# Kernel optimization log

Measured on AMD Instinct MI355X. Metric: run time of the kernel, lower is better.

The kernel has to match this reference:

```python
import jax, jax.numpy as jnp
import numpy as np

N = 50000      # nodes
E = 800000     # edges (avg degree 16)
DIN = 128
DH = 128
DOUT = 8


def setup_inputs() -> dict:
    key = jax.random.key(0)
    ks = jax.random.split(key, 9)
    def lin(k, o, i):
        return (jax.random.normal(k, (o, i), jnp.float32) / np.sqrt(i)).astype(jnp.float32)
    return {
        "x": jax.random.normal(ks[0], (N, DIN), jnp.float32),
        "edge_index": jax.random.randint(ks[1], (2, E), 0, N),
        "edge_attr": jax.random.normal(ks[2], (E, 1), jnp.float32),
        # SAGEConv params: lin_l (applied to mean-aggregated neighbors, with bias)
        # and lin_r (applied to root node, no bias), per PyG defaults.
        "W1l": lin(ks[3], DH, DIN), "b1l": jnp.zeros((DH,), jnp.float32), "W1r": lin(ks[4], DH, DIN),
        "Whl": lin(ks[5], DH, DH),  "bhl": jnp.zeros((DH,), jnp.float32), "Whr": lin(ks[6], DH, DH),
        "W2l": lin(ks[7], DOUT, DH), "b2l": jnp.zeros((DOUT,), jnp.float32), "W2r": lin(ks[8], DOUT, DH),
    }


def _sage_conv(x, src, dst, Wl, bl, Wr, n):
    # mean aggregation of source features onto destination nodes
    s = jax.ops.segment_sum(x[src], dst, num_segments=n)              # [N, d]
    c = jax.ops.segment_sum(jnp.ones((src.shape[0],), x.dtype), dst, num_segments=n)
    agg = s / jnp.maximum(c, 1.0)[:, None]
    return agg @ Wl.T + bl + x @ Wr.T


def reference(x, edge_index, edge_attr, W1l, b1l, W1r, Whl, bhl, Whr, W2l, b2l, W2r):
    # edge_attr is accepted but unused, matching the original forward.
    src, dst = edge_index[0], edge_index[1]
    n = x.shape[0]
    h = jax.nn.relu(_sage_conv(x, src, dst, W1l, b1l, W1r, n))
    # dropout p=0.5 is identity at inference (training=False)
    h = jax.nn.elu(_sage_conv(h, src, dst, Whl, bhl, Whr, n))
    h = _sage_conv(h, src, dst, W2l, b2l, W2r, n)
    return jax.nn.log_softmax(h, axis=1)
```

## Files before the change

### kernel.cpp

```cpp
#include <hip/hip_runtime.h>

typedef unsigned int u32;
typedef unsigned short u16;
typedef short bf16x8 __attribute__((ext_vector_type(8)));
typedef float f32x4 __attribute__((ext_vector_type(4)));

#define NCB 256

__device__ __forceinline__ float bf2f(u16 h) { return __uint_as_float(((u32)h) << 16); }
__device__ __forceinline__ u16 f2bf(float f) {
    u32 u = __float_as_uint(f);
    return (u16)((u + 0x7fffu + ((u >> 16) & 1u)) >> 16);
}

__global__ __launch_bounds__(256) void k_sentinel(u16* out, int n) {
    int i = blockIdx.x * 256 + threadIdx.x;
    if (i < n) out[i] = f2bf(-7.0f);
}

__global__ void k_detect(const u32* x, int* flag) {
    int lane = threadIdx.x;
    int c = 0;
    for (int j = 0; j < 4; ++j) {
        u32 u = x[lane * 4 + j];
        u32 e = (u >> 7) & 0xffu;
        if ((e >= 0x30u && e <= 0x47u) || ((u & 0x7fffu) == 0u)) ++c;
    }
    for (int d = 32; d; d >>= 1) c += __shfl_down(c, d, 64);
    if (lane == 0) *flag = (c < 128) ? 1 : 0;
}

__global__ __launch_bounds__(256) void k_front(
    const void* x, const int* dstv, const int* flag, int bucketed,
    uint4* X, int* C, int E, int N, int chunk, int cvtB,
    const void* s1l, const void* s1r, const void* shl, const void* shr,
    const void* s2l, const void* s2r, const void* sb1, const void* sbh,
    const void* sb2,
    u32* w1l, u32* w1r, u32* whl, u32* whr, u32* w2l, u32* w2r,
    float* bf1, float* bfh, float* bf2) {
    __shared__ int hist[256];
    int b = blockIdx.x, t = threadIdx.x;
    if (b < cvtB) {
        int i = b * 256 + t;
        if (i >= N * 16) return;
        if (*flag) {
            const float4* s = (const float4*)x;
            float4 a = s[2 * i], c4 = s[2 * i + 1];
            uint4 o;
            o.x = (u32)f2bf(a.x) | ((u32)f2bf(a.y) << 16);
            o.y = (u32)f2bf(a.z) | ((u32)f2bf(a.w) << 16);
            o.z = (u32)f2bf(c4.x) | ((u32)f2bf(c4.y) << 16);
            o.w = (u32)f2bf(c4.z) | ((u32)f2bf(c4.w) << 16);
            X[i] = o;
        } else {
            X[i] = ((const uint4*)x)[i];
        }
    } else if (b < cvtB + 134) {
        int bb = b - cvtB;
        int fl = *flag;
        auto cv = [&](const void* src, u32* dst, int base) {
            int i = base + t;
            if (fl) {
                const float* s = (const float*)src;
                dst[i] = (u32)f2bf(s[2 * i]) | ((u32)f2bf(s[2 * i + 1]) << 16);
            } else {
                dst[i] = ((const u32*)src)[i];
            }
        };
        auto cb = [&](const void* src, float* dst, int i) {
            dst[i] = fl ? ((const float*)src)[i] : bf2f(((const u16*)src)[i]);
        };
        if      (bb <  32) cv(s1l, w1l, bb * 256);
        else if (bb <  64) cv(s1r, w1r, (bb - 32) * 256);
        else if (bb <  96) cv(shl, whl, (bb - 64) * 256);
        else if (bb < 128) cv(shr, whr, (bb - 96) * 256);
        else if (bb < 130) cv(s2l, w2l, (bb - 128) * 256);
        else if (bb < 132) cv(s2r, w2r, (bb - 130) * 256);
        else if (bb == 132) {
            if (t < 128) cb(sb1, bf1, t);
            else         cb(sbh, bfh, t - 128);
        } else {
            if (t < 8) cb(sb2, bf2, t);
        }
    } else if (bucketed) {
        int cb2 = b - cvtB - 134;
        hist[t] = 0;
        __syncthreads();
        int e0 = cb2 * chunk;
        int e1 = min(e0 + chunk, E);
        for (int e = e0 + t; e < e1; e += 256) {
            int d = min(max(dstv[e], 0), N - 1);
            atomicAdd(&hist[d >> 8], 1);
        }
        __syncthreads();
        C[cb2 * 256 + t] = hist[t];
    }
}

__global__ __launch_bounds__(256) void k_scanT(int* C, int* T) {
    __shared__ int sm[256];
    int bu = blockIdx.x, t = threadIdx.x;
    int v = C[t * 256 + bu];
    sm[t] = v;
    __syncthreads();
    for (int off = 1; off < 256; off <<= 1) {
        int u = (t >= off) ? sm[t - off] : 0;
        __syncthreads();
        sm[t] += u;
        __syncthreads();
    }
    C[t * 256 + bu] = sm[t] - v;
    if (t == 255) T[bu] = sm[255];
}

__global__ __launch_bounds__(256) void k_scanB(const int* T, int* B, int nbuk) {
    __shared__ int sm[256];
    int t = threadIdx.x;
    int v = (t < nbuk) ? T[t] : 0;
    sm[t] = v;
    __syncthreads();
    for (int off = 1; off < 256; off <<= 1) {
        int u = (t >= off) ? sm[t - off] : 0;
        __syncthreads();
        sm[t] += u;
        __syncthreads();
    }
    B[t] = sm[t] - v;
}

__global__ __launch_bounds__(256) void k_place(const int* srcv, const int* dstv,
                                               const int* C, const int* Bb,
                                               u32* pairs, int E, int N, int chunk) {
    __shared__ int base[256], cnt[256];
    int t = threadIdx.x;
    base[t] = Bb[t] + C[blockIdx.x * 256 + t];
    cnt[t] = 0;
    __syncthreads();
    int e0 = blockIdx.x * chunk;
    int e1 = min(e0 + chunk, E);
    for (int e = e0 + t; e < e1; e += 256) {
        int d = min(max(dstv[e], 0), N - 1);
        int s = min(max(srcv[e], 0), N - 1);
        int b = d >> 8;
        int pos = base[b] + atomicAdd(&cnt[b], 1);
        pos = min(max(pos, 0), E - 1);
        pairs[pos] = ((u32)s << 8) | (u32)(d & 255);
    }
}

__global__ __launch_bounds__(256) void k_fillb2(const u32* pairs, const int* Bb,
                                                const int* T, int* rowptr,
                                                int* adj, int E, int N, int nbuk) {
    int bu = blockIdx.x;
    int n0 = bu << 8;
    int nn = min(N - n0, 256);
    __shared__ int dcnt[256], sm[256], cur[256];
    int t = threadIdx.x;
    dcnt[t] = 0;
    __syncthreads();
    int s0 = min(max(Bb[bu], 0), E);
    int s1 = min(s0 + max(T[bu], 0), E);
    for (int e = s0 + t; e < s1; e += 256) {
        int ld = (int)(pairs[e] & 255u);
        atomicAdd(&dcnt[min(ld, nn - 1)], 1);
    }
    __syncthreads();
    int v = dcnt[t];
    sm[t] = v;
    __syncthreads();
    for (int off = 1; off < 256; off <<= 1) {
        int u = (t >= off) ? sm[t - off] : 0;
        __syncthreads();
        sm[t] += u;
        __syncthreads();
    }
    int excl = sm[t] - v;
    cur[t] = excl;
    if (t < nn) rowptr[n0 + t] = s0 + excl;
    if (bu == nbuk - 1 && t == 0) rowptr[N] = E;
    __syncthreads();
    for (int e = s0 + t; e < s1; e += 256) {
        u32 pc = pairs[e];
        int ld = min((int)(pc & 255u), nn - 1);
        int src = (int)(pc >> 8);
        int slot = atomicAdd(&cur[ld], 1);
        int idx = min(max(s0 + slot, 0), E - 1);
        adj[idx] = src;
    }
}

__global__ __launch_bounds__(256) void k_zero(int* deg, int N) {
    int i = blockIdx.x * 256 + threadIdx.x;
    if (i < N) deg[i] = 0;
}
__global__ __launch_bounds__(256) void k_deg(const int* dstv, int* deg, int E, int N) {
    int e = blockIdx.x * 256 + threadIdx.x;
    if (e >= E) return;
    int d = dstv[e]; d = min(max(d, 0), N - 1);
    atomicAdd(&deg[d], 1);
}
__global__ __launch_bounds__(512) void k_scan1(const int* deg, int* r0,
                                               int* bsums, int N) {
    __shared__ int sm[512];
    int i = blockIdx.x * 512 + threadIdx.x;
    int v = (i < N) ? deg[i] : 0;
    sm[threadIdx.x] = v;
    __syncthreads();
    for (int off = 1; off < 512; off <<= 1) {
        int t = (threadIdx.x >= off) ? sm[threadIdx.x - off] : 0;
        __syncthreads();
        sm[threadIdx.x] += t;
        __syncthreads();
    }
    if (i < N) r0[i] = sm[threadIdx.x] - v;
    if (threadIdx.x == 511) bsums[blockIdx.x] = sm[511];
}
__global__ __launch_bounds__(128) void k_scan2f(int* bsums, int nb) {
    __shared__ int sm[128];
    int v = (threadIdx.x < nb) ? bsums[threadIdx.x] : 0;
    sm[threadIdx.x] = v;
    __syncthreads();
    for (int off = 1; off < 128; off <<= 1) {
        int t = (threadIdx.x >= off) ? sm[threadIdx.x - off] : 0;
        __syncthreads();
        sm[threadIdx.x] += t;
        __syncthreads();
    }
    if (threadIdx.x < nb) bsums[threadIdx.x] = sm[threadIdx.x] - v;
}
__global__ __launch_bounds__(512) void k_scan3f(const int* r0, const int* bsums,
                                                int* rowptr, int N, int E) {
    int i = blockIdx.x * 512 + threadIdx.x;
    if (i < N) rowptr[i] = r0[i] + bsums[blockIdx.x];
    if (i == 0) rowptr[N] = E;
}
__global__ __launch_bounds__(256) void k_fill(const int* srcv, const int* dstv,
                                              const int* rowptr, int* deg,
                                              int* adj, int E, int N) {
    int e = blockIdx.x * 256 + threadIdx.x;
    if (e >= E) return;
    int d = dstv[e]; d = min(max(d, 0), N - 1);
    int slot = atomicSub(&deg[d], 1) - 1;
    int idx = rowptr[d] + slot;
    idx = min(max(idx, 0), E - 1);
    adj[idx] = srcv[e];
}

__device__ __forceinline__ void acc8m(uint4 u, float m, float* s) {
    const u32* pu = (const u32*)&u;
#pragma unroll
    for (int t = 0; t < 4; ++t) {
        s[2 * t]     = fmaf(__uint_as_float(pu[t] << 16), m, s[2 * t]);
        s[2 * t + 1] = fmaf(__uint_as_float(pu[t] & 0xffff0000u), m, s[2 * t + 1]);
    }
}

__global__ __launch_bounds__(256) void k_aggregate(const uint4* F, const int* rowptr,
                                                   const int* adj, uint4* A,
                                                   int N, int E) {
    int wid = (int)((blockIdx.x * 256u + threadIdx.x) >> 6);
    int lane = threadIdx.x & 63;
    if (wid >= N) return;
    int beg = rowptr[wid], end = rowptr[wid + 1];
    beg = min(max(beg, 0), E);
    end = min(max(end, beg), E);
    int g = lane >> 4, l = lane & 15;
    float s[8] = {0.f, 0.f, 0.f, 0.f, 0.f, 0.f, 0.f, 0.f};
    for (int j = beg + g; j < end; j += 16) {
        int i1 = j + 4, i2 = j + 8, i3 = j + 12;
        float m1 = (i1 < end) ? 1.f : 0.f;
        float m2 = (i2 < end) ? 1.f : 0.f;
        float m3 = (i3 < end) ? 1.f : 0.f;
        int a0 = min(max(adj[j], 0), N - 1);
        int a1 = min(max(adj[min(i1, end - 1)], 0), N - 1);
        int a2 = min(max(adj[min(i2, end - 1)], 0), N - 1);
        int a3 = min(max(adj[min(i3, end - 1)], 0), N - 1);
        uint4 u0 = F[(size_t)a0 * 16 + l];
        uint4 u1 = F[(size_t)a1 * 16 + l];
        uint4 u2 = F[(size_t)a2 * 16 + l];
        uint4 u3 = F[(size_t)a3 * 16 + l];
        acc8m(u0, 1.f, s);
        acc8m(u1, m1, s);
        acc8m(u2, m2, s);
        acc8m(u3, m3, s);
    }
#pragma unroll
    for (int k = 0; k < 8; ++k) {
        s[k] += __shfl_xor(s[k], 16, 64);
        s[k] += __shfl_xor(s[k], 32, 64);
    }
    if (g == 0) {
        float inv = 1.f / fmaxf((float)(end - beg), 1.f);
        uint4 r; u32* pr = (u32*)&r;
#pragma unroll
        for (int t = 0; t < 4; ++t)
            pr[t] = (u32)f2bf(s[2 * t] * inv) | ((u32)f2bf(s[2 * t + 1] * inv) << 16);
        A[(size_t)wid * 16 + l] = r;
    }
}

__global__ __launch_bounds__(256) void k_gemm128(const u16* Agg, const u16* Xin,
                                                 const u32* Wl, const u32* Wr,
                                                 const float* bias, u16* Out, int N) {
    __shared__ __align__(16) u16 Wsh[32768];
    int t = threadIdx.x;
#pragma unroll
    for (int i = 0; i < 16; ++i) {
        int f = i * 256 + t;
        int c = f >> 9, s = (f >> 6) & 7, q = (f >> 4) & 3, n = f & 15;
        int o = c * 16 + n;
        int k = s * 32 + q * 8;
        uint4 v;
        if (k < 128) v = *(const uint4*)(Wl + (size_t)o * 64 + (k >> 1));
        else         v = *(const uint4*)(Wr + (size_t)o * 64 + ((k - 128) >> 1));
        *(uint4*)(Wsh + f * 8) = v;
    }
    __syncthreads();

    int tile = blockIdx.x * 4 + (t >> 6);
    int lane = t & 63;
    int m0 = tile * 16;
    if (m0 >= N) return;
    int mrow = min(m0 + (lane & 15), N - 1);
    int kq = (lane >> 4) * 8;

    bf16x8 afrag[8];
#pragma unroll
    for (int s = 0; s < 8; ++s) {
        int k = s * 32 + kq;
        const u16* p = (k < 128) ? (Agg + (size_t)mrow * 128 + k)
                                 : (Xin + (size_t)mrow * 128 + (k - 128));
        afrag[s] = *(const bf16x8*)p;
    }

    f32x4 acc[8];
#pragma unroll
    for (int c = 0; c < 8; ++c) acc[c] = (f32x4){0.f, 0.f, 0.f, 0.f};

    const u16* lbase = Wsh + (lane >> 4) * 128 + (lane & 15) * 8;
#pragma unroll
    for (int c = 0; c < 8; ++c) {
#pragma unroll
        for (int s = 0; s < 8; ++s) {
            bf16x8 b = *(const bf16x8*)(lbase + (c * 8 + s) * 512);
            acc[c] = __builtin_amdgcn_mfma_f32_16x16x32_bf16(afrag[s], b, acc[c], 0, 0, 0);
        }
    }

#pragma unroll
    for (int c = 0; c < 8; ++c) {
        int o = c * 16 + (lane & 15);
        float bv = bias[o];
#pragma unroll
        for (int r = 0; r < 4; ++r) {
            int m = m0 + (lane >> 4) * 4 + r;
            float v = acc[c][r] + bv;
            v = fmaxf(v, 0.f);
            if (m < N) Out[(size_t)m * 128 + o] = f2bf(v);
        }
    }
}

__global__ __launch_bounds__(256) void k_gemm2(const u16* Agg, const u16* Xin,
                                               const u32* Wl, const u32* Wr,
                                               const float* bias,
                                               const u32* W2l, const u32* W2r,
                                               const float* b2,
                                               float* Y, float* R, int N) {
    __shared__ __align__(16) u16 Wsh[32768];
    __shared__ float W2sh[2048];
    int t = threadIdx.x;
#pragma unroll
    for (int i = 0; i < 16; ++i) {
        int f = i * 256 + t;
        int c = f >> 9, s = (f >> 6) & 7, q = (f >> 4) & 3, n = f & 15;
        int o = c * 16 + n;
        int k = s * 32 + q * 8;
        uint4 v;
        if (k < 128) v = *(const uint4*)(Wl + (size_t)o * 64 + (k >> 1));
        else         v = *(const uint4*)(Wr + (size_t)o * 64 + ((k - 128) >> 1));
        *(uint4*)(Wsh + f * 8) = v;
    }
#pragma unroll
    for (int i = t; i < 512; i += 256) {
        u32 wa = W2l[i], wb = W2r[i];
        W2sh[2 * i]            = bf2f((u16)(wa & 0xffffu));
        W2sh[2 * i + 1]        = bf2f((u16)(wa >> 16));
        W2sh[1024 + 2 * i]     = bf2f((u16)(wb & 0xffffu));
        W2sh[1024 + 2 * i + 1] = bf2f((u16)(wb >> 16));
    }
    __syncthreads();

    int tile = blockIdx.x * 4 + (t >> 6);
    int lane = t & 63;
    int m0 = tile * 16;
    if (m0 >= N) return;
    int mrow = min(m0 + (lane & 15), N - 1);
    int kq = (lane >> 4) * 8;

    bf16x8 afrag[8];
#pragma unroll
    for (int s = 0; s < 8; ++s) {
        int k = s * 32 + kq;
        const u16* p = (k < 128) ? (Agg + (size_t)mrow * 128 + k)
                                 : (Xin + (size_t)mrow * 128 + (k - 128));
        afrag[s] = *(const bf16x8*)p;
    }

    f32x4 acc[8];
#pragma unroll
    for (int c = 0; c < 8; ++c) acc[c] = (f32x4){0.f, 0.f, 0.f, 0.f};

    const u16* lbase = Wsh + (lane >> 4) * 128 + (lane & 15) * 8;
#pragma unroll
    for (int c = 0; c < 8; ++c) {
#pragma unroll
        for (int s = 0; s < 8; ++s) {
            bf16x8 b = *(const bf16x8*)(lbase + (c * 8 + s) * 512);
            acc[c] = __builtin_amdgcn_mfma_f32_16x16x32_bf16(afrag[s], b, acc[c], 0, 0, 0);
        }
    }

    int quad = lane >> 4, k15 = lane & 15;
#pragma unroll
    for (int c = 0; c < 8; ++c) {
        float bv = bias[c * 16 + k15];
#pragma unroll
        for (int r = 0; r < 4; ++r) {
            float v = acc[c][r] + bv;
            acc[c][r] = (v > 0.f) ? v : expm1f(v);
        }
    }

    bool b0 = (k15 & 1) != 0, b1 = (k15 & 2) != 0, b2v = (k15 & 4) != 0;
    int jm = 4 * (k15 & 1) + (k15 & 2) + ((k15 >> 2) & 1);
#pragma unroll
    for (int r = 0; r < 4; ++r) {
        float pj[8], qj[8];
#pragma unroll
        for (int j = 0; j < 8; ++j) { pj[j] = 0.f; qj[j] = 0.f; }
#pragma unroll
        for (int c = 0; c < 8; ++c) {
            float av = acc[c][r];
#pragma unroll
            for (int j = 0; j < 8; ++j) {
                pj[j] = fmaf(av, W2sh[j * 128 + c * 16 + k15], pj[j]);
                qj[j] = fmaf(av, W2sh[1024 + j * 128 + c * 16 + k15], qj[j]);
            }
        }
        float p4[4], q4[4];
#pragma unroll
        for (int j = 0; j < 4; ++j) {
            float ps = b0 ? pj[j] : pj[j + 4];
            float qs = b0 ? qj[j] : qj[j + 4];
            p4[j] = (b0 ? pj[j + 4] : pj[j]) + __shfl_xor(ps, 1, 64);
            q4[j] = (b0 ? qj[j + 4] : qj[j]) + __shfl_xor(qs, 1, 64);
        }
        float p2[2], q2[2];
#pragma unroll
        for (int j = 0; j < 2; ++j) {
            float ps = b1 ? p4[j] : p4[j + 2];
            float qs = b1 ? q4[j] : q4[j + 2];
            p2[j] = (b1 ? p4[j + 2] : p4[j]) + __shfl_xor(ps, 2, 64);
            q2[j] = (b1 ? q4[j + 2] : q4[j]) + __shfl_xor(qs, 2, 64);
        }
        float ps = b2v ? p2[0] : p2[1];
        float qs = b2v ? q2[0] : q2[1];
        float pv = (b2v ? p2[1] : p2[0]) + __shfl_xor(ps, 4, 64);
        float qv = (b2v ? q2[1] : q2[0]) + __shfl_xor(qs, 4, 64);
        pv += __shfl_xor(pv, 8, 64);
        qv += __shfl_xor(qv, 8, 64);
        int m = m0 + quad * 4 + r;
        if (m < N) {
            if (k15 < 8) Y[(size_t)m * 8 + jm] = pv;
            else         R[(size_t)m * 8 + jm] = qv + b2[jm];
        }
    }
}

__global__ __launch_bounds__(256) void k_agg8sm(const float* Y, const float* R,
                                                const int* rowptr, const int* adj,
                                                const int* flag, void* Out,
                                                int N, int E) {
    int t = blockIdx.x * 256 + threadIdx.x;
    int n = t >> 3;
    int o = t & 7;
    if (n >= N) return;
    int beg = rowptr[n], end = rowptr[n + 1];
    beg = min(max(beg, 0), E);
    end = min(max(end, beg), E);
    float s = 0.f;
    int j = beg;
    for (; j + 1 < end; j += 2) {
        int a0 = min(max(adj[j], 0), N - 1);
        int a1 = min(max(adj[j + 1], 0), N - 1);
        s += Y[(size_t)a0 * 8 + o];
        s += Y[(size_t)a1 * 8 + o];
    }
    if (j < end) {
        int a0 = min(max(adj[j], 0), N - 1);
        s += Y[(size_t)a0 * 8 + o];
    }
    float acc = s / fmaxf((float)(end - beg), 1.f) + R[(size_t)n * 8 + o];
    float mx = acc;
#pragma unroll
    for (int d = 1; d < 8; d <<= 1) mx = fmaxf(mx, __shfl_xor(mx, d, 64));
    float ex = expf(acc - mx), se = ex;
#pragma unroll
    for (int d = 1; d < 8; d <<= 1) se += __shfl_xor(se, d, 64);
    float v = acc - mx - logf(se);
    if (*flag) ((float*)Out)[(size_t)n * 8 + o] = v;
    else       ((u16*)Out)[(size_t)n * 8 + o] = f2bf(v);
}

extern "C" void kernel_launch(void* const* d_in, const int* in_sizes, int n_in,
                              void* d_out, int out_size, void* d_ws, size_t ws_size,
                              hipStream_t stream) {
    const void* x   = d_in[0];
    const int* ei   = (const int*)d_in[1];
    const int N = in_sizes[0] / 128;
    const int E = in_sizes[1] / 2;
    const int* srcv = ei;
    const int* dstv = ei + E;
    const int NBUK = (N + 255) >> 8;
    const int bucketed = (NBUK <= 256) ? 1 : 0;
    const int chunk = (E + NCB - 1) / NCB;
    const int cvtB = (N * 16 + 255) / 256;
    const int nbA = (N + 511) / 512;

    auto rnd = [](size_t b) { return (b + 255) & ~(size_t)255; };
    size_t need = rnd(256)
                + rnd((size_t)N * 4)
                + rnd((size_t)N * 4)
                + rnd((size_t)(N + 1) * 4)
                + rnd(4096)
                + rnd(256 * NCB * 4)
                + rnd(1024) + rnd(1024)
                + rnd((size_t)E * 4)
                + 2 * rnd((size_t)N * 256)
                + 2 * rnd((size_t)N * 32)
                + 4 * rnd(32768) + 2 * rnd(2048) + 2 * rnd(512) + rnd(64);
    if (ws_size < need) {
        k_sentinel<<<(out_size + 255) / 256, 256, 0, stream>>>((u16*)d_out, out_size);
        return;
    }

    char* p = (char*)d_ws;
    auto carve = [&](size_t bytes) { char* r = p; p += (bytes + 255) & ~(size_t)255; return r; };
    int* flag   = (int*)carve(256);
    int* deg    = (int*)carve((size_t)N * 4);
    int* r0     = (int*)carve((size_t)N * 4);
    int* rowptr = (int*)carve((size_t)(N + 1) * 4);
    int* bsums  = (int*)carve(4096);
    int* C      = (int*)carve(256 * NCB * 4);
    int* T      = (int*)carve(1024);
    int* B      = (int*)carve(1024);
    int* adj    = (int*)carve((size_t)E * 4);
    u32* X      = (u32*)carve((size_t)N * 256);
    u32* A      = (u32*)carve((size_t)N * 256);
    float* Y    = (float*)carve((size_t)N * 32);
    float* R    = (float*)carve((size_t)N * 32);
    u32* w1l = (u32*)carve(32768); u32* w1r = (u32*)carve(32768);
    u32* whl = (u32*)carve(32768); u32* whr = (u32*)carve(32768);
    u32* w2l = (u32*)carve(2048);  u32* w2r = (u32*)carve(2048);
    float* bf1 = (float*)carve(512); float* bfh = (float*)carve(512);
    float* bf2 = (float*)carve(64);
    u32* pairs = A;
    (void)n_in;

    k_detect<<<1, 64, 0, stream>>>((const u32*)x, flag);
    k_front<<<cvtB + 134 + (bucketed ? 256 : 0), 256, 0, stream>>>(
        x, dstv, flag, bucketed, (uint4*)X, C, E, N, chunk, cvtB,
        d_in[3], d_in[5], d_in[6], d_in[8], d_in[9], d_in[11],
        d_in[4], d_in[7], d_in[10],
        w1l, w1r, whl, whr, w2l, w2r, bf1, bfh, bf2);
    if (bucketed) {
        k_scanT<<<NBUK, 256, 0, stream>>>(C, T);
        k_scanB<<<1, 256, 0, stream>>>(T, B, NBUK);
        k_place<<<NCB, 256, 0, stream>>>(srcv, dstv, C, B, pairs, E, N, chunk);
        k_fillb2<<<NBUK, 256, 0, stream>>>(pairs, B, T, rowptr, adj, E, N, NBUK);
    } else {
        k_zero<<<(N + 255) / 256, 256, 0, stream>>>(deg, N);
        k_deg<<<(E + 255) / 256, 256, 0, stream>>>(dstv, deg, E, N);
        k_scan1<<<nbA, 512, 0, stream>>>(deg, r0, bsums, N);
        k_scan2f<<<1, 128, 0, stream>>>(bsums, nbA);
        k_scan3f<<<nbA, 512, 0, stream>>>(r0, bsums, rowptr, N, E);
        k_fill<<<(E + 255) / 256, 256, 0, stream>>>(srcv, dstv, rowptr, deg, adj, E, N);
    }

    int aggBlocks = (int)(((size_t)N * 64 + 255) / 256);
    int gemmBlocks = ((N + 15) / 16 + 3) / 4;
    int perNode8 = (int)(((size_t)N * 8 + 255) / 256);

    k_aggregate<<<aggBlocks, 256, 0, stream>>>((const uint4*)X, rowptr, adj, (uint4*)A, N, E);
    k_gemm128<<<gemmBlocks, 256, 0, stream>>>((const u16*)A, (const u16*)X, w1l, w1r, bf1, (u16*)X, N);
    k_aggregate<<<aggBlocks, 256, 0, stream>>>((const uint4*)X, rowptr, adj, (uint4*)A, N, E);
    k_gemm2<<<gemmBlocks, 256, 0, stream>>>((const u16*)A, (const u16*)X, whl, whr, bfh,
                                            w2l, w2r, bf2, Y, R, N);
    k_agg8sm<<<perNode8, 256, 0, stream>>>(Y, R, rowptr, adj, flag, d_out, N, E);
}
```

Baseline: 244.5 us.

## Fold dtype detection into front kernel, widen GEMM blocks, unroll final gather

```diff
diff --git a/kernel.cpp b/kernel.cpp
--- a/kernel.cpp
+++ b/kernel.cpp
@@ -18,20 +18,8 @@
     if (i < n) out[i] = f2bf(-7.0f);
 }
 
-__global__ void k_detect(const u32* x, int* flag) {
-    int lane = threadIdx.x;
-    int c = 0;
-    for (int j = 0; j < 4; ++j) {
-        u32 u = x[lane * 4 + j];
-        u32 e = (u >> 7) & 0xffu;
-        if ((e >= 0x30u && e <= 0x47u) || ((u & 0x7fffu) == 0u)) ++c;
-    }
-    for (int d = 32; d; d >>= 1) c += __shfl_down(c, d, 64);
-    if (lane == 0) *flag = (c < 128) ? 1 : 0;
-}
-
 __global__ __launch_bounds__(256) void k_front(
-    const void* x, const int* dstv, const int* flag, int bucketed,
+    const void* x, const int* dstv, int* flagOut, int bucketed,
     uint4* X, int* C, int E, int N, int chunk, int cvtB,
     const void* s1l, const void* s1r, const void* shl, const void* shr,
     const void* s2l, const void* s2r, const void* sb1, const void* sbh,
@@ -39,11 +27,26 @@
     u32* w1l, u32* w1r, u32* whl, u32* whr, u32* w2l, u32* w2r,
     float* bf1, float* bfh, float* bf2) {
     __shared__ int hist[256];
+    __shared__ int sflag;
     int b = blockIdx.x, t = threadIdx.x;
+    if (t < 64) {
+        int c = 0;
+        for (int j = 0; j < 4; ++j) {
+            u32 u = ((const u32*)x)[t * 4 + j];
+            u32 e = (u >> 7) & 0xffu;
+            if ((e >= 0x30u && e <= 0x47u) || ((u & 0x7fffu) == 0u)) ++c;
+        }
+        for (int d = 32; d; d >>= 1) c += __shfl_down(c, d, 64);
+        if (t == 0) sflag = (c < 128) ? 1 : 0;
+    }
+    __syncthreads();
+    int fl = sflag;
+    if (b == 0 && t == 0) *flagOut = fl;
+
     if (b < cvtB) {
         int i = b * 256 + t;
         if (i >= N * 16) return;
-        if (*flag) {
+        if (fl) {
             const float4* s = (const float4*)x;
             float4 a = s[2 * i], c4 = s[2 * i + 1];
             uint4 o;
@@ -57,7 +60,6 @@
         }
     } else if (b < cvtB + 134) {
         int bb = b - cvtB;
-        int fl = *flag;
         auto cv = [&](const void* src, u32* dst, int base) {
             int i = base + t;
             if (fl) {
@@ -299,14 +301,14 @@
     }
 }
 
-__global__ __launch_bounds__(256) void k_gemm128(const u16* Agg, const u16* Xin,
+__global__ __launch_bounds__(512) void k_gemm128(const u16* Agg, const u16* Xin,
                                                  const u32* Wl, const u32* Wr,
                                                  const float* bias, u16* Out, int N) {
     __shared__ __align__(16) u16 Wsh[32768];
     int t = threadIdx.x;
 #pragma unroll
-    for (int i = 0; i < 16; ++i) {
-        int f = i * 256 + t;
+    for (int i = 0; i < 8; ++i) {
+        int f = i * 512 + t;
         int c = f >> 9, s = (f >> 6) & 7, q = (f >> 4) & 3, n = f & 15;
         int o = c * 16 + n;
         int k = s * 32 + q * 8;
@@ -317,7 +319,7 @@
     }
     __syncthreads();
 
-    int tile = blockIdx.x * 4 + (t >> 6);
+    int tile = blockIdx.x * 8 + (t >> 6);
     int lane = t & 63;
     int m0 = tile * 16;
     if (m0 >= N) return;
@@ -361,7 +363,7 @@
     }
 }
 
-__global__ __launch_bounds__(256) void k_gemm2(const u16* Agg, const u16* Xin,
+__global__ __launch_bounds__(512) void k_gemm2(const u16* Agg, const u16* Xin,
                                                const u32* Wl, const u32* Wr,
                                                const float* bias,
                                                const u32* W2l, const u32* W2r,
@@ -371,8 +373,8 @@
     __shared__ float W2sh[2048];
     int t = threadIdx.x;
 #pragma unroll
-    for (int i = 0; i < 16; ++i) {
-        int f = i * 256 + t;
+    for (int i = 0; i < 8; ++i) {
+        int f = i * 512 + t;
         int c = f >> 9, s = (f >> 6) & 7, q = (f >> 4) & 3, n = f & 15;
         int o = c * 16 + n;
         int k = s * 32 + q * 8;
@@ -381,17 +383,16 @@
         else         v = *(const uint4*)(Wr + (size_t)o * 64 + ((k - 128) >> 1));
         *(uint4*)(Wsh + f * 8) = v;
     }
-#pragma unroll
-    for (int i = t; i < 512; i += 256) {
-        u32 wa = W2l[i], wb = W2r[i];
-        W2sh[2 * i]            = bf2f((u16)(wa & 0xffffu));
-        W2sh[2 * i + 1]        = bf2f((u16)(wa >> 16));
-        W2sh[1024 + 2 * i]     = bf2f((u16)(wb & 0xffffu));
-        W2sh[1024 + 2 * i + 1] = bf2f((u16)(wb >> 16));
-    }
-    __syncthreads();
-
-    int tile = blockIdx.x * 4 + (t >> 6);
+    if (t < 512) {
+        u32 wa = W2l[t], wb = W2r[t];
+        W2sh[2 * t]            = bf2f((u16)(wa & 0xffffu));
+        W2sh[2 * t + 1]        = bf2f((u16)(wa >> 16));
+        W2sh[1024 + 2 * t]     = bf2f((u16)(wb & 0xffffu));
+        W2sh[1024 + 2 * t + 1] = bf2f((u16)(wb >> 16));
+    }
+    __syncthreads();
+
+    int tile = blockIdx.x * 8 + (t >> 6);
     int lane = t & 63;
     int m0 = tile * 16;
     if (m0 >= N) return;
@@ -490,16 +491,23 @@
     beg = min(max(beg, 0), E);
     end = min(max(end, beg), E);
     float s = 0.f;
-    int j = beg;
-    for (; j + 1 < end; j += 2) {
+    for (int j = beg; j < end; j += 4) {
+        int j1 = j + 1, j2 = j + 2, j3 = j + 3;
+        float m1 = (j1 < end) ? 1.f : 0.f;
+        float m2 = (j2 < end) ? 1.f : 0.f;
+        float m3 = (j3 < end) ? 1.f : 0.f;
         int a0 = min(max(adj[j], 0), N - 1);
-        int a1 = min(max(adj[j + 1], 0), N - 1);
-        s += Y[(size_t)a0 * 8 + o];
-        s += Y[(size_t)a1 * 8 + o];
-    }
-    if (j < end) {
-        int a0 = min(max(adj[j], 0), N - 1);
-        s += Y[(size_t)a0 * 8 + o];
+        int a1 = min(max(adj[min(j1, end - 1)], 0), N - 1);
+        int a2 = min(max(adj[min(j2, end - 1)], 0), N - 1);
+        int a3 = min(max(adj[min(j3, end - 1)], 0), N - 1);
+        float y0 = Y[(size_t)a0 * 8 + o];
+        float y1 = Y[(size_t)a1 * 8 + o];
+        float y2 = Y[(size_t)a2 * 8 + o];
+        float y3 = Y[(size_t)a3 * 8 + o];
+        s += y0;
+        s = fmaf(y1, m1, s);
+        s = fmaf(y2, m2, s);
+        s = fmaf(y3, m3, s);
     }
     float acc = s / fmaxf((float)(end - beg), 1.f) + R[(size_t)n * 8 + o];
     float mx = acc;
@@ -568,7 +576,6 @@
     u32* pairs = A;
     (void)n_in;
 
-    k_detect<<<1, 64, 0, stream>>>((const u32*)x, flag);
     k_front<<<cvtB + 134 + (bucketed ? 256 : 0), 256, 0, stream>>>(
         x, dstv, flag, bucketed, (uint4*)X, C, E, N, chunk, cvtB,
         d_in[3], d_in[5], d_in[6], d_in[8], d_in[9], d_in[11],
@@ -589,13 +596,14 @@
     }
 
     int aggBlocks = (int)(((size_t)N * 64 + 255) / 256);
-    int gemmBlocks = ((N + 15) / 16 + 3) / 4;
+    int tiles = (N + 15) / 16;
+    int gemmBlocks = (tiles + 7) / 8;
     int perNode8 = (int)(((size_t)N * 8 + 255) / 256);
 
     k_aggregate<<<aggBlocks, 256, 0, stream>>>((const uint4*)X, rowptr, adj, (uint4*)A, N, E);
-    k_gemm128<<<gemmBlocks, 256, 0, stream>>>((const u16*)A, (const u16*)X, w1l, w1r, bf1, (u16*)X, N);
+    k_gemm128<<<gemmBlocks, 512, 0, stream>>>((const u16*)A, (const u16*)X, w1l, w1r, bf1, (u16*)X, N);
     k_aggregate<<<aggBlocks, 256, 0, stream>>>((const uint4*)X, rowptr, adj, (uint4*)A, N, E);
-    k_gemm2<<<gemmBlocks, 256, 0, stream>>>((const u16*)A, (const u16*)X, whl, whr, bfh,
+    k_gemm2<<<gemmBlocks, 512, 0, stream>>>((const u16*)A, (const u16*)X, whl, whr, bfh,
                                             w2l, w2r, bf2, Y, R, N);
     k_agg8sm<<<perNode8, 256, 0, stream>>>(Y, R, rowptr, adj, flag, d_out, N, E);
 }
```

Measured after the change: 225.6 us. 7.7% less time.
